# Kernel optimization log

Measured on AMD Instinct MI355X. Metric: run time of the kernel, lower is better.

Reference implementation:

```python
import jax, jax.numpy as jnp
import numpy as np
import math

D_MODEL = 1024
N_HEADS = 16
HEAD_DIM = D_MODEL // N_HEADS


def _compute_slopes(n_heads: int) -> np.ndarray:
    def pow2_slopes(n):
        start = 2.0 ** (-(2.0 ** (-(math.log2(n) - 3))))
        return [start * (start ** i) for i in range(n)]
    if math.log2(n_heads).is_integer():
        s = pow2_slopes(n_heads)
    else:
        cp = 2 ** math.floor(math.log2(n_heads))
        s = pow2_slopes(cp) + pow2_slopes(2 * cp)[0::2][: n_heads - cp]
    return np.asarray(s, dtype=np.float32)


def setup_inputs() -> dict:
    key = jax.random.key(0)
    ks = jax.random.split(key, 11)
    B, T, D = 2, 2048, D_MODEL
    scale = 1.0 / math.sqrt(D)
    inp = {
        "query": jax.random.normal(ks[0], (B, T, D), jnp.float32),
        "key": jax.random.normal(ks[1], (B, T, D), jnp.float32),
        "value": jax.random.normal(ks[2], (B, T, D), jnp.float32),
        "Wq": jax.random.normal(ks[3], (D, D), jnp.float32) * scale,
        "bq": jnp.zeros((D,), jnp.float32),
        "Wk": jax.random.normal(ks[4], (D, D), jnp.float32) * scale,
        "bk": jnp.zeros((D,), jnp.float32),
        "Wv": jax.random.normal(ks[5], (D, D), jnp.float32) * scale,
        "bv": jnp.zeros((D,), jnp.float32),
        "Wo": jax.random.normal(ks[6], (D, D), jnp.float32) * scale,
        "bo": jnp.zeros((D,), jnp.float32),
    }
    return inp


def reference(query, key, value, Wq, bq, Wk, bk, Wv, bv, Wo, bo):
    B, Tq, D = query.shape
    Tk = key.shape[1]
    H, hd = N_HEADS, HEAD_DIM
    scale = hd ** -0.5

    # projections -> [B, H, T, hd]
    Q = (query @ Wq + bq).reshape(B, Tq, H, hd).transpose(0, 2, 1, 3)
    K = (key @ Wk + bk).reshape(B, Tk, H, hd).transpose(0, 2, 1, 3)
    V = (value @ Wv + bv).reshape(B, Tk, H, hd).transpose(0, 2, 1, 3)

    # scores [B, H, Tq, Tk]
    attn = jnp.einsum("bhqd,bhkd->bhqk", Q, K) * scale

    # ALiBi bias (only applied when Tq == Tk, mirroring the original)
    slopes = jnp.asarray(_compute_slopes(H))  # [H]
    pos = jnp.arange(Tq)
    dist = -jnp.abs(pos[None, :] - pos[:, None]).astype(jnp.float32)  # [Tq, Tk]
    bias = slopes[:, None, None] * dist[None]  # [H, Tq, Tk]
    attn = attn + bias[None]

    attn = jax.nn.softmax(attn, axis=-1)
    out = jnp.einsum("bhqk,bhkd->bhqd", attn, V)
    out = out.transpose(0, 2, 1, 3).reshape(B, Tq, D)
    return out @ Wo + bo
```

## Files before the change

kernel.cpp:

```cpp
#include <hip/hip_runtime.h>
#include <stdint.h>

#define BSZ 2
#define TT 2048
#define DD 1024
#define HH 16
#define HD 64

typedef __bf16 bf16x8 __attribute__((ext_vector_type(8)));
typedef float f32x4 __attribute__((ext_vector_type(4)));

#if __has_builtin(__builtin_amdgcn_exp2f)
__device__ __forceinline__ float fexp2(float x) { return __builtin_amdgcn_exp2f(x); }
#else
__device__ __forceinline__ float fexp2(float x) {
    float r; asm("v_exp_f32 %0, %1\n\ts_nop 1" : "=v"(r) : "v"(x)); return r;
}
#endif

__device__ __forceinline__ unsigned short f2bf(float f) {
    union { float f; unsigned u; } c; c.f = f;
    unsigned u = c.u;
    unsigned r = u + 0x7fffu + ((u >> 16) & 1u);
    return (unsigned short)(r >> 16);
}
__device__ __forceinline__ unsigned fasu(float f) {
    union { float f; unsigned u; } c; c.f = f; return c.u;
}

union U4BF { uint4 u; bf16x8 b; };
__device__ __forceinline__ bf16x8 as_bf8(uint4 v) { U4BF c; c.u = v; return c.b; }

#if __has_builtin(__builtin_amdgcn_global_load_lds)
__device__ __forceinline__ void gl_lds16(const ushort* g, ushort* l) {
    __builtin_amdgcn_global_load_lds(
        (const __attribute__((address_space(1))) uint32_t*)g,
        (__attribute__((address_space(3))) uint32_t*)l, 16, 0, 0);
}
#define GLL_LANE 1
#else
__device__ __forceinline__ void gl_lds16_fallback(const ushort* g, ushort* l, int lane) {
    *(uint4*)(l + lane * 8) = *(const uint4*)(g);
}
#define GLL_LANE 0
#endif

__global__ __launch_bounds__(256)
void prep(const float* __restrict__ q, const float* __restrict__ k,
          const float* __restrict__ v,
          const float* __restrict__ W0, const float* __restrict__ W1,
          const float* __restrict__ W2, const float* __restrict__ W3,
          ushort* __restrict__ xq, ushort* __restrict__ xk, ushort* __restrict__ xv,
          ushort* __restrict__ T0, ushort* __restrict__ T1,
          ushort* __restrict__ T2, ushort* __restrict__ T3) {
    __shared__ float sh[32][33];
    const int y = blockIdx.y;
    if (y < 3) {
        const float* in = (y == 0) ? q : (y == 1) ? k : v;
        ushort* out = (y == 0) ? xq : (y == 1) ? xk : xv;
        int i = blockIdx.x * 256 + threadIdx.x;
        float4 val = ((const float4*)in)[i];
        ushort4 o;
        o.x = f2bf(val.x); o.y = f2bf(val.y); o.z = f2bf(val.z); o.w = f2bf(val.w);
        ((ushort4*)out)[i] = o;
    } else {
        const int x = blockIdx.x;
        const float* src; ushort* dst;
        switch (x >> 10) {
            case 0:  src = W0; dst = T0; break;
            case 1:  src = W1; dst = T1; break;
            case 2:  src = W2; dst = T2; break;
            default: src = W3; dst = T3; break;
        }
        const int tile = x & 1023;
        const int k0 = (tile >> 5) * 32, n0 = (tile & 31) * 32;
        const int tx = threadIdx.x & 31, ty = threadIdx.x >> 5;
        #pragma unroll
        for (int p = 0; p < 4; ++p)
            sh[ty + 8 * p][tx] = src[(size_t)(k0 + ty + 8 * p) * DD + n0 + tx];
        __syncthreads();
        #pragma unroll
        for (int p = 0; p < 4; ++p)
            dst[(size_t)(n0 + ty + 8 * p) * DD + k0 + tx] = f2bf(sh[tx][ty + 8 * p]);
    }
}

__global__ __launch_bounds__(256)
void vtrans(const ushort* __restrict__ Vh, ushort* __restrict__ Vt) {
    __shared__ ushort sh[64][72];
    const int tid = threadIdx.x;
    const int bh = blockIdx.y;
    const int t0 = blockIdx.x * 64;
    const size_t base = (size_t)bh * (TT * HD);
    #pragma unroll
    for (int it = 0; it < 2; ++it) {
        int u = tid + it * 256;
        int r = u >> 3, c8 = (u & 7) * 8;
        *(uint4*)&sh[r][c8] = *(const uint4*)(Vh + base + (size_t)(t0 + r) * HD + c8);
    }
    __syncthreads();
    #pragma unroll
    for (int it = 0; it < 2; ++it) {
        int u = tid + it * 256;
        int d = u >> 3, c8 = (u & 7) * 8;
        alignas(16) ushort tmp[8];
        #pragma unroll
        for (int p = 0; p < 8; ++p) tmp[p] = sh[c8 + p][d];
        *(uint4*)(Vt + base + (size_t)d * TT + t0 + c8) = *(const uint4*)tmp;
    }
}

template<int BM, int OUT_MODE>
__global__ __launch_bounds__(256)
void gemm_mfma(const ushort* __restrict__ A0, const ushort* __restrict__ B0,
               const float* __restrict__ c0, void* __restrict__ d0,
               const ushort* __restrict__ A1, const ushort* __restrict__ B1,
               const float* __restrict__ c1, void* __restrict__ d1,
               const ushort* __restrict__ A2, const ushort* __restrict__ B2,
               const float* __restrict__ c2, void* __restrict__ d2) {
    constexpr int TI = 4;
    constexpr int TJ = (BM == 128) ? 4 : 2;
    constexpr int WC = (BM == 128) ? 2 : 4;
    __shared__ __attribute__((aligned(16))) ushort As[BM][32];
    __shared__ __attribute__((aligned(16))) ushort Bs[128][32];
    const ushort* A; const ushort* Bt; const float* bias; void* outp;
    switch (blockIdx.z) {
        case 0:  A = A0; Bt = B0; bias = c0; outp = d0; break;
        case 1:  A = A1; Bt = B1; bias = c1; outp = d1; break;
        default: A = A2; Bt = B2; bias = c2; outp = d2; break;
    }
    const int tid  = threadIdx.x;
    const int lane = tid & 63, w = tid >> 6;
    const int wr = w / WC, wc = w % WC;
    const int ln = lane & 15, quad = lane >> 4;
    const int m0 = blockIdx.y * BM, n0 = blockIdx.x * 128;

    const f32x4 zero = {0.f, 0.f, 0.f, 0.f};
    f32x4 acc[TI][TJ];
    #pragma unroll
    for (int i = 0; i < TI; ++i)
        #pragma unroll
        for (int j = 0; j < TJ; ++j) acc[i][j] = zero;

    const int lr  = lane >> 2;
    const int lc8 = (lane & 3) * 8;

    for (int kb = 0; kb < 1024; kb += 32) {
        #pragma unroll
        for (int it = 0; it < BM / 64; ++it) {
            int r0 = it * 64 + w * 16;
#if GLL_LANE
            gl_lds16(A + (size_t)(m0 + r0 + lr) * 1024 + kb + lc8, &As[r0][0]);
#else
            gl_lds16_fallback(A + (size_t)(m0 + r0 + lr) * 1024 + kb + lc8, &As[r0][0], lane);
#endif
        }
        #pragma unroll
        for (int it = 0; it < 2; ++it) {
            int r0 = it * 64 + w * 16;
#if GLL_LANE
            gl_lds16(Bt + (size_t)(n0 + r0 + lr) * 1024 + kb + lc8, &Bs[r0][0]);
#else
            gl_lds16_fallback(Bt + (size_t)(n0 + r0 + lr) * 1024 + kb + lc8, &Bs[r0][0], lane);
#endif
        }
        __syncthreads();
        bf16x8 af[TI], bfr[TJ];
        #pragma unroll
        for (int i = 0; i < TI; ++i)
            af[i] = as_bf8(*(const uint4*)&As[wr * 64 + i * 16 + ln][quad * 8]);
        #pragma unroll
        for (int j = 0; j < TJ; ++j)
            bfr[j] = as_bf8(*(const uint4*)&Bs[wc * (TJ * 16) + j * 16 + ln][quad * 8]);
        #pragma unroll
        for (int i = 0; i < TI; ++i)
            #pragma unroll
            for (int j = 0; j < TJ; ++j)
                acc[i][j] = __builtin_amdgcn_mfma_f32_16x16x32_bf16(af[i], bfr[j], acc[i][j], 0, 0, 0);
        __syncthreads();
    }

    #pragma unroll
    for (int j = 0; j < TJ; ++j) {
        int n = n0 + wc * (TJ * 16) + j * 16 + ln;
        float bv = bias[n];
        #pragma unroll
        for (int i = 0; i < TI; ++i) {
            #pragma unroll
            for (int r = 0; r < 4; ++r) {
                int m = m0 + wr * 64 + i * 16 + quad * 4 + r;
                float v = acc[i][j][r] + bv;
                if (OUT_MODE == 0) {
                    int b = m >> 11, t = m & 2047, h = n >> 6, d = n & 63;
                    ((ushort*)outp)[(((size_t)(b * HH + h)) * TT + t) * HD + d] = f2bf(v);
                } else {
                    ((float*)outp)[(size_t)m * 1024 + n] = v;
                }
            }
        }
    }
}

__global__ __launch_bounds__(256)
void attn_kernel(const ushort* __restrict__ Qh, const ushort* __restrict__ Kh,
                 const ushort* __restrict__ Vtg, ushort* __restrict__ outp) {
    __shared__ __attribute__((aligned(16))) char smem[33792];
    ushort (*Ps)[32][72] = (ushort (*)[32][72])smem;
    float  (*Rbuf)[64][44] = (float (*)[64][44])smem;

    const int tid  = threadIdx.x;
    const int lane = tid & 63, w = tid >> 6;
    const int ln = lane & 15, quad = lane >> 4;

    bf16x8 ones;
    {
        union { ushort us[8]; bf16x8 v; } uu;
        #pragma unroll
        for (int p = 0; p < 8; ++p) uu.us[p] = 0x3F80;
        ones = uu.v;
    }
    const f32x4 zero = {0.f, 0.f, 0.f, 0.f};
    const float c1 = 0.125f * 1.44269504f;

    for (int sel = 0; sel < 2; ++sel) {
        __syncthreads();
        const int item = sel ? (2047 - (int)blockIdx.x) : (int)blockIdx.x;
        const int h = 15 - (item >> 7);
        const int rr = item & 127;
        const int b = rr & 1;
        const int qt = rr >> 1;
        const int bh = b * 16 + h;
        const int qbase = qt * 32;
        const float slope2 = exp2f(-0.5f * (float)(h + 1)) * 1.44269504f;
        const size_t base = (size_t)bh * (TT * HD);

        const int D = (int)ceilf(18.0f / slope2);
        int lo = qbase - D;
        int kt_lo = (lo > 0) ? (lo >> 6) : 0;
        int kt_hi = (qbase + 32 + D + 63) >> 6;
        if (kt_hi > TT / 64) kt_hi = TT / 64;
        const int nt = kt_hi - kt_lo;
        const int cs = (nt + 3) >> 2;
        const int my_lo = kt_lo + w * cs;
        const int my_hi = (my_lo + cs < kt_hi) ? (my_lo + cs) : kt_hi;

        bf16x8 qa[2][2];
        #pragma unroll
        for (int g = 0; g < 2; ++g) {
            const uint4* qp = (const uint4*)(Qh + base + (size_t)(qbase + g * 16 + ln) * HD);
            qa[g][0] = as_bf8(qp[quad]);
            qa[g][1] = as_bf8(qp[4 + quad]);
        }
        f32x4 o[2][4], lsum[2];
        #pragma unroll
        for (int g = 0; g < 2; ++g) {
            lsum[g] = zero;
            #pragma unroll
            for (int dn = 0; dn < 4; ++dn) o[g][dn] = zero;
        }
        float qrf[2][4];
        #pragma unroll
        for (int g = 0; g < 2; ++g)
            #pragma unroll
            for (int r = 0; r < 4; ++r)
                qrf[g][r] = (float)(qbase + g * 16 + quad * 4 + r);

        const ushort* kp = Kh  + base + (size_t)ln * HD + quad * 8;
        const ushort* vp = Vtg + base + (size_t)ln * TT + quad * 8;

        if (my_lo < my_hi) {
            uint4 kf[8];
            {
                const int ko = my_lo * 4096;
                #pragma unroll
                for (int n = 0; n < 4; ++n)
                    #pragma unroll
                    for (int hf = 0; hf < 2; ++hf)
                        kf[n * 2 + hf] = *(const uint4*)(kp + ko + n * 1024 + hf * 32);
            }

            for (int kt = my_lo; kt < my_hi; ++kt) {
                uint4 vf[8];
                {
                    const int vo = kt * 64;
                    #pragma unroll
                    for (int dn = 0; dn < 4; ++dn)
                        #pragma unroll
                        for (int hf = 0; hf < 2; ++hf)
                            vf[dn * 2 + hf] = *(const uint4*)(vp + dn * 32768 + vo + hf * 32);
                }
                uint4 kn[8];
                if (kt + 1 < my_hi) {
                    const int ko = (kt + 1) * 4096;
                    #pragma unroll
                    for (int n = 0; n < 4; ++n)
                        #pragma unroll
                        for (int hf = 0; hf < 2; ++hf)
                            kn[n * 2 + hf] = *(const uint4*)(kp + ko + n * 1024 + hf * 32);
                }

                f32x4 s[2][4];
                #pragma unroll
                for (int n = 0; n < 4; ++n) {
                    bf16x8 b0 = as_bf8(kf[n * 2]);
                    bf16x8 b1 = as_bf8(kf[n * 2 + 1]);
                    #pragma unroll
                    for (int g = 0; g < 2; ++g) {
                        f32x4 zz = zero;
                        zz = __builtin_amdgcn_mfma_f32_16x16x32_bf16(qa[g][0], b0, zz, 0, 0, 0);
                        s[g][n] = __builtin_amdgcn_mfma_f32_16x16x32_bf16(qa[g][1], b1, zz, 0, 0, 0);
                    }
                }

                #pragma unroll
                for (int n = 0; n < 4; ++n) {
                    float kg = (float)(kt * 64 + n * 16 + ln);
                    int bswz = ((2 * n + (ln >> 3)) ^ quad) * 8 + (ln & 7);
                    #pragma unroll
                    for (int g = 0; g < 2; ++g) {
                        #pragma unroll
                        for (int r = 0; r < 4; ++r) {
                            float d = qrf[g][r] - kg;
                            float arg = fmaf(s[g][n][r], c1, -slope2 * fabsf(d));
                            float p = fexp2(arg);
                            Ps[w][g * 16 + quad * 4 + r][bswz] = (ushort)(fasu(p) >> 16);
                        }
                    }
                }

                #pragma unroll
                for (int hf = 0; hf < 2; ++hf) {
                    bf16x8 ap0 = as_bf8(*(const uint4*)&Ps[w][ln]     [((hf * 4 + quad) ^ (ln >> 2)) * 8]);
                    bf16x8 ap1 = as_bf8(*(const uint4*)&Ps[w][16 + ln][((hf * 4 + quad) ^ (ln >> 2)) * 8]);
                    #pragma unroll
                    for (int dn = 0; dn < 4; ++dn) {
                        bf16x8 bv = as_bf8(vf[dn * 2 + hf]);
                        o[0][dn] = __builtin_amdgcn_mfma_f32_16x16x32_bf16(ap0, bv, o[0][dn], 0, 0, 0);
                        o[1][dn] = __builtin_amdgcn_mfma_f32_16x16x32_bf16(ap1, bv, o[1][dn], 0, 0, 0);
                    }
                    lsum[0] = __builtin_amdgcn_mfma_f32_16x16x32_bf16(ap0, ones, lsum[0], 0, 0, 0);
                    lsum[1] = __builtin_amdgcn_mfma_f32_16x16x32_bf16(ap1, ones, lsum[1], 0, 0, 0);
                }

                #pragma unroll
                for (int i = 0; i < 8; ++i) kf[i] = kn[i];
            }
        }

        __syncthreads();
        if (w > 0) {
            float* dst = &Rbuf[w - 1][lane][0];
            #pragma unroll
            for (int g = 0; g < 2; ++g) {
                #pragma unroll
                for (int dn = 0; dn < 4; ++dn)
                    #pragma unroll
                    for (int r = 0; r < 4; ++r)
                        dst[g * 16 + dn * 4 + r] = o[g][dn][r];
                #pragma unroll
                for (int r = 0; r < 4; ++r)
                    dst[32 + g * 4 + r] = lsum[g][r];
            }
        }
        __syncthreads();
        if (w == 0) {
            #pragma unroll
            for (int j = 0; j < 3; ++j) {
                const float* src = &Rbuf[j][lane][0];
                #pragma unroll
                for (int g = 0; g < 2; ++g) {
                    #pragma unroll
                    for (int dn = 0; dn < 4; ++dn)
                        #pragma unroll
                        for (int r = 0; r < 4; ++r)
                            o[g][dn][r] += src[g * 16 + dn * 4 + r];
                    #pragma unroll
                    for (int r = 0; r < 4; ++r)
                        lsum[g][r] += src[32 + g * 4 + r];
                }
            }
            #pragma unroll
            for (int g = 0; g < 2; ++g) {
                #pragma unroll
                for (int r = 0; r < 4; ++r) {
                    float inv = __builtin_amdgcn_rcpf(lsum[g][r]);
                    int q = qbase + g * 16 + quad * 4 + r;
                    size_t ob = ((size_t)(b * TT + q)) * DD + h * HD;
                    #pragma unroll
                    for (int dn = 0; dn < 4; ++dn)
                        outp[ob + dn * 16 + ln] = f2bf(o[g][dn][r] * inv);
                }
            }
        }
    }
}

extern "C" void kernel_launch(void* const* d_in, const int* in_sizes, int n_in,
                              void* d_out, int out_size, void* d_ws, size_t ws_size,
                              hipStream_t stream) {
    const float* query = (const float*)d_in[0];
    const float* key   = (const float*)d_in[1];
    const float* value = (const float*)d_in[2];
    const float* Wq = (const float*)d_in[3];
    const float* bq = (const float*)d_in[4];
    const float* Wk = (const float*)d_in[5];
    const float* bk = (const float*)d_in[6];
    const float* Wv = (const float*)d_in[7];
    const float* bv = (const float*)d_in[8];
    const float* Wo = (const float*)d_in[9];
    const float* bo = (const float*)d_in[10];
    float* out = (float*)d_out;

    char* ws = (char*)d_ws;
    const size_t MB = 1024 * 1024;
    ushort* Xq  = (ushort*)(ws + 0);
    ushort* Xk  = (ushort*)(ws + 8 * MB);
    ushort* Xv  = (ushort*)(ws + 16 * MB);
    ushort* Wtq = (ushort*)(ws + 24 * MB);
    ushort* Wtk = (ushort*)(ws + 26 * MB);
    ushort* Wtv = (ushort*)(ws + 28 * MB);
    ushort* Wto = (ushort*)(ws + 30 * MB);
    ushort* Qh  = (ushort*)(ws + 32 * MB);
    ushort* Kh  = (ushort*)(ws + 40 * MB);
    ushort* Vh  = (ushort*)(ws + 48 * MB);
    ushort* Vt   = (ushort*)(ws + 16 * MB);
    ushort* attn = (ushort*)(ws + 0);

    prep<<<dim3(4096, 4), 256, 0, stream>>>(query, key, value, Wq, Wk, Wv, Wo,
                                            Xq, Xk, Xv, Wtq, Wtk, Wtv, Wto);

    gemm_mfma<128, 0><<<dim3(8, 32, 3), 256, 0, stream>>>(
        Xq, Wtq, bq, Qh,  Xk, Wtk, bk, Kh,  Xv, Wtv, bv, Vh);

    vtrans<<<dim3(TT / 64, BSZ * HH), 256, 0, stream>>>(Vh, Vt);

    attn_kernel<<<dim3(1024), 256, 0, stream>>>(Qh, Kh, Vt, attn);

    gemm_mfma<64, 1><<<dim3(8, 64, 1), 256, 0, stream>>>(
        attn, Wto, bo, out,  attn, Wto, bo, out,  attn, Wto, bo, out);
}
```

Measured before the change: 255.2 us.

## Fuse V transpose into projection epilogue and add atomic work queue for attention

The V projection GEMM now writes its output directly in transposed [bh][d][t] layout with packed 4-element stores, which removes the separate vtrans kernel and its round trip through memory. The attention kernel replaces its fixed two-items-per-block pairing with a dynamic work queue driven by an atomic counter. The counter lives in the output buffer, is initialised by prep, and is later overwritten by the final GEMM. This adds one atomic and two barriers per item and relies on kernels running in stream order for the counter reset.

```diff
diff --git a/kernel.cpp b/kernel.cpp
--- a/kernel.cpp
+++ b/kernel.cpp
@@ -52,7 +52,8 @@
           const float* __restrict__ W2, const float* __restrict__ W3,
           ushort* __restrict__ xq, ushort* __restrict__ xk, ushort* __restrict__ xv,
           ushort* __restrict__ T0, ushort* __restrict__ T1,
-          ushort* __restrict__ T2, ushort* __restrict__ T3) {
+          ushort* __restrict__ T2, ushort* __restrict__ T3,
+          int* __restrict__ ctr) {
     __shared__ float sh[32][33];
     const int y = blockIdx.y;
     if (y < 3) {
@@ -64,6 +65,7 @@
         o.x = f2bf(val.x); o.y = f2bf(val.y); o.z = f2bf(val.z); o.w = f2bf(val.w);
         ((ushort4*)out)[i] = o;
     } else {
+        if (blockIdx.x == 0 && threadIdx.x == 0) *ctr = 1024;
         const int x = blockIdx.x;
         const float* src; ushort* dst;
         switch (x >> 10) {
@@ -82,31 +84,6 @@
         #pragma unroll
         for (int p = 0; p < 4; ++p)
             dst[(size_t)(n0 + ty + 8 * p) * DD + k0 + tx] = f2bf(sh[tx][ty + 8 * p]);
-    }
-}
-
-__global__ __launch_bounds__(256)
-void vtrans(const ushort* __restrict__ Vh, ushort* __restrict__ Vt) {
-    __shared__ ushort sh[64][72];
-    const int tid = threadIdx.x;
-    const int bh = blockIdx.y;
-    const int t0 = blockIdx.x * 64;
-    const size_t base = (size_t)bh * (TT * HD);
-    #pragma unroll
-    for (int it = 0; it < 2; ++it) {
-        int u = tid + it * 256;
-        int r = u >> 3, c8 = (u & 7) * 8;
-        *(uint4*)&sh[r][c8] = *(const uint4*)(Vh + base + (size_t)(t0 + r) * HD + c8);
-    }
-    __syncthreads();
-    #pragma unroll
-    for (int it = 0; it < 2; ++it) {
-        int u = tid + it * 256;
-        int d = u >> 3, c8 = (u & 7) * 8;
-        alignas(16) ushort tmp[8];
-        #pragma unroll
-        for (int p = 0; p < 8; ++p) tmp[p] = sh[c8 + p][d];
-        *(uint4*)(Vt + base + (size_t)d * TT + t0 + c8) = *(const uint4*)tmp;
     }
 }
 
@@ -124,7 +101,8 @@
     __shared__ __attribute__((aligned(16))) ushort As[BM][32];
     __shared__ __attribute__((aligned(16))) ushort Bs[128][32];
     const ushort* A; const ushort* Bt; const float* bias; void* outp;
-    switch (blockIdx.z) {
+    const int z = blockIdx.z;
+    switch (z) {
         case 0:  A = A0; Bt = B0; bias = c0; outp = d0; break;
         case 1:  A = A1; Bt = B1; bias = c1; outp = d1; break;
         default: A = A2; Bt = B2; bias = c2; outp = d2; break;
@@ -186,15 +164,26 @@
         float bv = bias[n];
         #pragma unroll
         for (int i = 0; i < TI; ++i) {
-            #pragma unroll
-            for (int r = 0; r < 4; ++r) {
-                int m = m0 + wr * 64 + i * 16 + quad * 4 + r;
-                float v = acc[i][j][r] + bv;
-                if (OUT_MODE == 0) {
-                    int b = m >> 11, t = m & 2047, h = n >> 6, d = n & 63;
-                    ((ushort*)outp)[(((size_t)(b * HH + h)) * TT + t) * HD + d] = f2bf(v);
-                } else {
-                    ((float*)outp)[(size_t)m * 1024 + n] = v;
+            int mb = m0 + wr * 64 + i * 16 + quad * 4;
+            if (OUT_MODE == 0 && z == 2) {
+                int b = mb >> 11, t = mb & 2047, h = n >> 6, d = n & 63;
+                ushort4 pk;
+                pk.x = f2bf(acc[i][j][0] + bv);
+                pk.y = f2bf(acc[i][j][1] + bv);
+                pk.z = f2bf(acc[i][j][2] + bv);
+                pk.w = f2bf(acc[i][j][3] + bv);
+                *(ushort4*)((ushort*)outp + ((size_t)((b * HH + h) * HD + d)) * TT + t) = pk;
+            } else {
+                #pragma unroll
+                for (int r = 0; r < 4; ++r) {
+                    int m = mb + r;
+                    float v = acc[i][j][r] + bv;
+                    if (OUT_MODE == 0) {
+                        int b = m >> 11, t = m & 2047, h = n >> 6, d = n & 63;
+                        ((ushort*)outp)[(((size_t)(b * HH + h)) * TT + t) * HD + d] = f2bf(v);
+                    } else {
+                        ((float*)outp)[(size_t)m * 1024 + n] = v;
+                    }
                 }
             }
         }
@@ -203,8 +192,10 @@
 
 __global__ __launch_bounds__(256)
 void attn_kernel(const ushort* __restrict__ Qh, const ushort* __restrict__ Kh,
-                 const ushort* __restrict__ Vtg, ushort* __restrict__ outp) {
+                 const ushort* __restrict__ Vtg, ushort* __restrict__ outp,
+                 int* __restrict__ ctr) {
     __shared__ __attribute__((aligned(16))) char smem[33792];
+    __shared__ int s_item;
     ushort (*Ps)[32][72] = (ushort (*)[32][72])smem;
     float  (*Rbuf)[64][44] = (float (*)[64][44])smem;
 
@@ -222,9 +213,8 @@
     const f32x4 zero = {0.f, 0.f, 0.f, 0.f};
     const float c1 = 0.125f * 1.44269504f;
 
-    for (int sel = 0; sel < 2; ++sel) {
-        __syncthreads();
-        const int item = sel ? (2047 - (int)blockIdx.x) : (int)blockIdx.x;
+    int item = blockIdx.x;
+    while (item < 2048) {
         const int h = 15 - (item >> 7);
         const int rr = item & 127;
         const int b = rr & 1;
@@ -392,6 +382,11 @@
                 }
             }
         }
+
+        __syncthreads();
+        if (tid == 0) s_item = atomicAdd(ctr, 1);
+        __syncthreads();
+        item = s_item;
     }
 }
 
@@ -422,19 +417,17 @@
     ushort* Wto = (ushort*)(ws + 30 * MB);
     ushort* Qh  = (ushort*)(ws + 32 * MB);
     ushort* Kh  = (ushort*)(ws + 40 * MB);
-    ushort* Vh  = (ushort*)(ws + 48 * MB);
-    ushort* Vt   = (ushort*)(ws + 16 * MB);
+    ushort* Vt  = (ushort*)(ws + 48 * MB);
     ushort* attn = (ushort*)(ws + 0);
+    int* ctr = (int*)d_out;
 
     prep<<<dim3(4096, 4), 256, 0, stream>>>(query, key, value, Wq, Wk, Wv, Wo,
-                                            Xq, Xk, Xv, Wtq, Wtk, Wtv, Wto);
+                                            Xq, Xk, Xv, Wtq, Wtk, Wtv, Wto, ctr);
 
     gemm_mfma<128, 0><<<dim3(8, 32, 3), 256, 0, stream>>>(
-        Xq, Wtq, bq, Qh,  Xk, Wtk, bk, Kh,  Xv, Wtv, bv, Vh);
-
-    vtrans<<<dim3(TT / 64, BSZ * HH), 256, 0, stream>>>(Vh, Vt);
-
-    attn_kernel<<<dim3(1024), 256, 0, stream>>>(Qh, Kh, Vt, attn);
+        Xq, Wtq, bq, Qh,  Xk, Wtk, bk, Kh,  Xv, Wtv, bv, Vt);
+
+    attn_kernel<<<dim3(1024), 256, 0, stream>>>(Qh, Kh, Vt, attn, ctr);
 
     gemm_mfma<64, 1><<<dim3(8, 64, 1), 256, 0, stream>>>(
         attn, Wto, bo, out,  attn, Wto, bo, out,  attn, Wto, bo, out);
```

Measured after the change: 243.0 us. 1.05x faster.
